# Kernel optimization log

Hardware: AMD Instinct MI355X
Metric: run time of the kernel (lower is better)

## Reference

```python
import jax, jax.numpy as jnp
import numpy as np
import math

VOCAB = 32000
D_MODEL = 1024
N_HEADS = 16
D_FF = 4096
N_LAYERS = 4
MAX_LEN = 2048
BATCH = 2
SEQ = 1024


def _sinusoidal_pe(max_len, d_model):
    pos = np.arange(max_len, dtype=np.float32)[:, None]
    div = np.exp(np.arange(0, d_model, 2, dtype=np.float32) * (-math.log(10000.0) / d_model))
    pe = np.zeros((max_len, d_model), dtype=np.float32)
    pe[:, 0::2] = np.sin(pos * div)
    pe[:, 1::2] = np.cos(pos * div)
    return jnp.asarray(pe)


def setup_inputs() -> dict:
    key = jax.random.key(0)
    ks = jax.random.split(key, 16)
    std = 0.02
    L, d, ff, V = N_LAYERS, D_MODEL, D_FF, VOCAB
    inp = {
        "input_ids": jax.random.randint(ks[0], (BATCH, SEQ), 0, V, dtype=jnp.int32),
        "tok_emb": jax.random.normal(ks[1], (V, d), jnp.float32) * std,
        "pe": _sinusoidal_pe(MAX_LEN, d),
        "Wq": jax.random.normal(ks[2], (L, d, d), jnp.float32) * std,
        "Wk": jax.random.normal(ks[3], (L, d, d), jnp.float32) * std,
        "Wv": jax.random.normal(ks[4], (L, d, d), jnp.float32) * std,
        "Wo": jax.random.normal(ks[5], (L, d, d), jnp.float32) * std,
        "bo": jnp.zeros((L, d), jnp.float32),
        "W1": jax.random.normal(ks[6], (L, d, ff), jnp.float32) * std,
        "b1": jnp.zeros((L, ff), jnp.float32),
        "W2": jax.random.normal(ks[7], (L, ff, d), jnp.float32) * std,
        "b2": jnp.zeros((L, d), jnp.float32),
        "ln1_g": jnp.ones((L, d), jnp.float32),
        "ln1_b": jnp.zeros((L, d), jnp.float32),
        "ln2_g": jnp.ones((L, d), jnp.float32),
        "ln2_b": jnp.zeros((L, d), jnp.float32),
        "lnf_g": jnp.ones((d,), jnp.float32),
        "lnf_b": jnp.zeros((d,), jnp.float32),
        "Whead": jax.random.normal(ks[8], (V, d), jnp.float32) * std,
    }
    return inp


def _layernorm(x, g, b, eps=1e-5):
    mu = jnp.mean(x, axis=-1, keepdims=True)
    var = jnp.var(x, axis=-1, keepdims=True)
    return (x - mu) * jax.lax.rsqrt(var + eps) * g + b


def reference(input_ids, tok_emb, pe, Wq, Wk, Wv, Wo, bo, W1, b1, W2, b2,
              ln1_g, ln1_b, ln2_g, ln2_b, lnf_g, lnf_b, Whead):
    B, S = input_ids.shape
    d, H = D_MODEL, N_HEADS
    dk = d // H
    scale = math.sqrt(dk)

    x = tok_emb[input_ids] * math.sqrt(d) + pe[:S][None, :, :]  # [B,S,d]
    causal = jnp.tril(jnp.ones((S, S), dtype=bool))  # [S,S]

    for l in range(N_LAYERS):
        # --- attention sub-block (pre-LN) ---
        h = _layernorm(x, ln1_g[l], ln1_b[l])
        q = (h @ Wq[l]).reshape(B, S, H, dk).transpose(0, 2, 1, 3)  # [B,H,S,dk]
        k = (h @ Wk[l]).reshape(B, S, H, dk).transpose(0, 2, 1, 3)
        v = (h @ Wv[l]).reshape(B, S, H, dk).transpose(0, 2, 1, 3)
        scores = jnp.einsum('bhqd,bhkd->bhqk', q, k) / scale  # [B,H,S,S]
        scores = jnp.where(causal[None, None], scores, -1e9)
        attn = jax.nn.softmax(scores, axis=-1)
        ctx = jnp.einsum('bhqk,bhkd->bhqd', attn, v)  # [B,H,S,dk]
        ctx = ctx.transpose(0, 2, 1, 3).reshape(B, S, d)
        x = x + ctx @ Wo[l] + bo[l]
        # --- feed-forward sub-block ---
        h = _layernorm(x, ln2_g[l], ln2_b[l])
        x = x + jax.nn.relu(h @ W1[l] + b1[l]) @ W2[l] + b2[l]

    x = _layernorm(x, lnf_g, lnf_b)
    logits = x @ Whead.T  # [B,S,V]
    return logits
```

## Files before the change

kernel.cpp:

```cpp
#include <hip/hip_runtime.h>
#include <stdint.h>

typedef unsigned short u16;
typedef unsigned int   u32;

#define D_MODEL 1024
#define NHEADS  16
#define DKH     64
#define DFF     4096
#define NLAYERS 4
#define BATCH   2
#define SEQ     1024
#define NTOK    (BATCH*SEQ)
#define NVOCAB  32000
#define QKV_LD  3072

typedef __bf16 bf16x8 __attribute__((ext_vector_type(8)));
typedef float  f32x4  __attribute__((ext_vector_type(4)));
typedef u32    u32x4  __attribute__((ext_vector_type(4)));

static __device__ __forceinline__ u16 f2bf(float f){
    union { float f; u32 u; } v; v.f = f;
    return (u16)((v.u + 0x7fffu + ((v.u >> 16) & 1u)) >> 16);
}
static __device__ __forceinline__ u32 pk2(float lo, float hi){
    return (u32)f2bf(lo) | ((u32)f2bf(hi) << 16);
}
static __device__ __forceinline__ bf16x8 ldb8(const u16* p){
    return *reinterpret_cast<const bf16x8*>(p);
}
static __device__ __forceinline__ f32x4 mfma16(bf16x8 a, bf16x8 b, f32x4 c){
    return __builtin_amdgcn_mfma_f32_16x16x32_bf16(a, b, c, 0, 0, 0);
}
static __device__ __forceinline__ void gld16(const void* g, void* l){
    __builtin_amdgcn_global_load_lds((__attribute__((address_space(1))) u32*)g,
                                     (__attribute__((address_space(3))) u32*)l, 16, 0, 0);
}

__global__ __launch_bounds__(256) void k_embed(const int* __restrict__ ids,
        const float* __restrict__ tok, const float* __restrict__ pe,
        float* __restrict__ x){
    int t = blockIdx.x;
    int c = threadIdx.x * 4;
    int id = ids[t];
    int s = t & (SEQ - 1);
    float4 tv = *(const float4*)(tok + (size_t)id * D_MODEL + c);
    float4 pv = *(const float4*)(pe  + (size_t)s  * D_MODEL + c);
    float4 o;
    o.x = tv.x * 32.0f + pv.x;
    o.y = tv.y * 32.0f + pv.y;
    o.z = tv.z * 32.0f + pv.z;
    o.w = tv.w * 32.0f + pv.w;
    *(float4*)(x + (size_t)t * D_MODEL + c) = o;
}

__global__ __launch_bounds__(256) void k_ln(const float* __restrict__ x,
        const float* __restrict__ g, const float* __restrict__ b,
        u16* __restrict__ out){
    int t = blockIdx.x;
    int tid = threadIdx.x;
    float4 v = *(const float4*)(x + (size_t)t * D_MODEL + tid * 4);
    float s  = v.x + v.y + v.z + v.w;
    float ss = v.x*v.x + v.y*v.y + v.z*v.z + v.w*v.w;
    #pragma unroll
    for (int off = 1; off < 64; off <<= 1){
        s  += __shfl_xor(s, off);
        ss += __shfl_xor(ss, off);
    }
    __shared__ float rs[4], rss[4];
    int w = tid >> 6;
    if ((tid & 63) == 0){ rs[w] = s; rss[w] = ss; }
    __syncthreads();
    s  = rs[0] + rs[1] + rs[2] + rs[3];
    ss = rss[0] + rss[1] + rss[2] + rss[3];
    float mu  = s * (1.0f / D_MODEL);
    float var = ss * (1.0f / D_MODEL) - mu * mu;
    float rstd = rsqrtf(var + 1e-5f);
    float4 gg = *(const float4*)(g + tid * 4);
    float4 bb = *(const float4*)(b + tid * 4);
    uint2 pkv;
    pkv.x = pk2((v.x - mu) * rstd * gg.x + bb.x, (v.y - mu) * rstd * gg.y + bb.y);
    pkv.y = pk2((v.z - mu) * rstd * gg.z + bb.z, (v.w - mu) * rstd * gg.w + bb.w);
    *(uint2*)(out + (size_t)t * D_MODEL + tid * 4) = pkv;
}

__global__ __launch_bounds__(256) void k_ln_acc(float* __restrict__ x,
        const float* __restrict__ p0, const float* __restrict__ p1,
        const float* __restrict__ bias,
        const float* __restrict__ g, const float* __restrict__ b,
        u16* __restrict__ out){
    int t = blockIdx.x;
    int tid = threadIdx.x;
    size_t idx = (size_t)t * D_MODEL + tid * 4;
    float4 v  = *(const float4*)(x + idx);
    float4 a0 = *(const float4*)(p0 + idx);
    float4 a1 = *(const float4*)(p1 + idx);
    float4 bv = *(const float4*)(bias + tid * 4);
    v.x += a0.x + a1.x + bv.x;
    v.y += a0.y + a1.y + bv.y;
    v.z += a0.z + a1.z + bv.z;
    v.w += a0.w + a1.w + bv.w;
    *(float4*)(x + idx) = v;
    float s  = v.x + v.y + v.z + v.w;
    float ss = v.x*v.x + v.y*v.y + v.z*v.z + v.w*v.w;
    #pragma unroll
    for (int off = 1; off < 64; off <<= 1){
        s  += __shfl_xor(s, off);
        ss += __shfl_xor(ss, off);
    }
    __shared__ float rs[4], rss[4];
    int w = tid >> 6;
    if ((tid & 63) == 0){ rs[w] = s; rss[w] = ss; }
    __syncthreads();
    s  = rs[0] + rs[1] + rs[2] + rs[3];
    ss = rss[0] + rss[1] + rss[2] + rss[3];
    float mu  = s * (1.0f / D_MODEL);
    float var = ss * (1.0f / D_MODEL) - mu * mu;
    float rstd = rsqrtf(var + 1e-5f);
    float4 gg = *(const float4*)(g + tid * 4);
    float4 bb = *(const float4*)(b + tid * 4);
    uint2 pkv;
    pkv.x = pk2((v.x - mu) * rstd * gg.x + bb.x, (v.y - mu) * rstd * gg.y + bb.y);
    pkv.y = pk2((v.z - mu) * rstd * gg.z + bb.z, (v.w - mu) * rstd * gg.w + bb.w);
    *(uint2*)(out + idx) = pkv;
}

__global__ __launch_bounds__(256) void k_cast(const float* __restrict__ in,
        u16* __restrict__ out){
    size_t i = ((size_t)blockIdx.x * 256 + threadIdx.x) * 8;
    float4 a = *(const float4*)(in + i);
    float4 b = *(const float4*)(in + i + 4);
    u32x4 o;
    o.x = pk2(a.x, a.y); o.y = pk2(a.z, a.w);
    o.z = pk2(b.x, b.y); o.w = pk2(b.z, b.w);
    *(u32x4*)(out + i) = o;
}

__global__ __launch_bounds__(256) void k_tconv_fused(
        const float* __restrict__ Wq, const float* __restrict__ Wk,
        const float* __restrict__ Wv, const float* __restrict__ Wo,
        const float* __restrict__ W1, const float* __restrict__ W2,
        u16* __restrict__ wqkvT, u16* __restrict__ woT,
        u16* __restrict__ w1T,   u16* __restrict__ w2T){
    __shared__ float tile[32][33];
    const int id = blockIdx.x;
    const float* in; u16* outp; int R, C, bx, by;
    if (id < 4096){
        int wsel = id >> 10, t = id & 1023;
        bx = t & 31; by = t >> 5; R = 1024; C = 1024;
        in   = (wsel == 0) ? Wq : (wsel == 1) ? Wk : (wsel == 2) ? Wv : Wo;
        outp = (wsel < 3) ? wqkvT + wsel * 1024 * 1024 : woT;
    } else if (id < 8192){
        int t = id - 4096; bx = t & 127; by = t >> 7;
        R = 1024; C = 4096; in = W1; outp = w1T;
    } else {
        int t = id - 8192; bx = t & 31; by = t >> 5;
        R = 4096; C = 1024; in = W2; outp = w2T;
    }
    const int tx = threadIdx.x & 31, ty = threadIdx.x >> 5;
    #pragma unroll
    for (int i = 0; i < 4; i++){
        int r = by * 32 + ty + i * 8;
        tile[ty + i * 8][tx] = in[(size_t)r * C + bx * 32 + tx];
    }
    __syncthreads();
    #pragma unroll
    for (int i = 0; i < 4; i++){
        int c = bx * 32 + ty + i * 8;
        outp[(size_t)c * R + by * 32 + tx] = f2bf(tile[tx][ty + i * 8]);
    }
}

__global__ __launch_bounds__(256) void k_vt(const u16* __restrict__ qkv,
        u16* __restrict__ vt){
    __shared__ u16 tile[32][33];
    int sb = blockIdx.x;
    int yz = blockIdx.y;
    int db = yz & 1;
    int bh = yz >> 1;
    int b = bh >> 4, h = bh & 15;
    int tx = threadIdx.x & 31, ty = threadIdx.x >> 5;
    #pragma unroll
    for (int i = 0; i < 4; i++){
        int s = sb * 32 + ty + i * 8;
        tile[ty + i * 8][tx] = qkv[(size_t)(b * SEQ + s) * QKV_LD + 2048 + h * DKH + db * 32 + tx];
    }
    __syncthreads();
    #pragma unroll
    for (int i = 0; i < 4; i++){
        int dh = db * 32 + ty + i * 8;
        vt[(size_t)(bh * DKH + dh) * SEQ + sb * 32 + tx] = tile[tx][ty + i * 8];
    }
}

template<bool BIAS, bool RELU, bool OBF16, bool AXISM>
__global__ __launch_bounds__(256, 2) void k_gemm128p(
    const u16* __restrict__ A, const u16* __restrict__ Bt,
    const float* __restrict__ bias,
    float* __restrict__ outF, u16* __restrict__ outH,
    int N, int Kfull, int NXT, int NMT, int NZ)
{
    __shared__ __align__(16) u16 lds[32768];
    const int bid = blockIdx.x;
    const int xcd = bid & 7;
    const int r   = bid >> 3;
    int m_t, n_t, z;
    if constexpr (AXISM) {
        const int mper = NMT >> 3;
        n_t = r % NXT;
        int r2 = r / NXT;
        z = r2 % NZ;
        m_t = xcd * mper + r2 / NZ;
    } else {
        const int nper = NXT >> 3;
        n_t = xcd * nper + r % nper;
        int r2 = r / nper;
        m_t = r2 % NMT;
        z = r2 / NMT;
    }
    const int m0 = m_t * 128;
    const int n0 = n_t * 128;
    const int Kz = Kfull / NZ;
    const int kbeg = z * Kz;
    const int NT = Kz >> 6;

    const int tid  = threadIdx.x;
    const int w    = tid >> 6;
    const int lane = tid & 63;
    const int wr   = w >> 1, wc = w & 1;
    const int lrow = lane & 15, lkg = lane >> 4;

    const int srow = tid >> 3;
    const int ssw  = ((tid & 7) ^ (srow & 7)) * 8;
    const u16* aSrc0 = A  + (size_t)(m0 +  0 + srow) * Kfull + kbeg + ssw;
    const u16* aSrc1 = A  + (size_t)(m0 + 32 + srow) * Kfull + kbeg + ssw;
    const u16* aSrc2 = A  + (size_t)(m0 + 64 + srow) * Kfull + kbeg + ssw;
    const u16* aSrc3 = A  + (size_t)(m0 + 96 + srow) * Kfull + kbeg + ssw;
    const u16* bSrc0 = Bt + (size_t)(n0 +  0 + srow) * Kfull + kbeg + ssw;
    const u16* bSrc1 = Bt + (size_t)(n0 + 32 + srow) * Kfull + kbeg + ssw;
    const u16* bSrc2 = Bt + (size_t)(n0 + 64 + srow) * Kfull + kbeg + ssw;
    const u16* bSrc3 = Bt + (size_t)(n0 + 96 + srow) * Kfull + kbeg + ssw;

    const int sw0 = ((0 + lkg) ^ (lrow & 7)) * 8;
    const int sw1 = ((4 + lkg) ^ (lrow & 7)) * 8;
    const int aBase = (wr * 64 + lrow) * 64;
    const int bBase = (wc * 64 + lrow) * 64 + 8192;

    f32x4 acc[4][4] = {};

    #define STAGE(s, st) do { \
        u16* ab_ = lds + (s) * 16384 + w * 512; \
        const int ko_ = (st) * 64; \
        gld16(aSrc0 + ko_, ab_);              \
        gld16(aSrc1 + ko_, ab_ + 2048);       \
        gld16(aSrc2 + ko_, ab_ + 4096);       \
        gld16(aSrc3 + ko_, ab_ + 6144);       \
        gld16(bSrc0 + ko_, ab_ + 8192);       \
        gld16(bSrc1 + ko_, ab_ + 10240);      \
        gld16(bSrc2 + ko_, ab_ + 12288);      \
        gld16(bSrc3 + ko_, ab_ + 14336);      \
    } while (0)

    STAGE(0, 0);
    STAGE(1, 1);
    asm volatile("s_waitcnt vmcnt(8)" ::: "memory");
    __builtin_amdgcn_s_barrier();
    __builtin_amdgcn_sched_barrier(0);

    for (int t = 0; t < NT; ++t){
        const int s = t & 1;
        const u16* As = lds + s * 16384;

        bf16x8 af0[4], bf0[4];
        #pragma unroll
        for (int i = 0; i < 4; i++) af0[i] = ldb8(As + aBase + i * 1024 + sw0);
        #pragma unroll
        for (int j = 0; j < 4; j++) bf0[j] = ldb8(As + bBase + j * 1024 + sw0);
        __builtin_amdgcn_s_setprio(1);
        #pragma unroll
        for (int i = 0; i < 4; i++)
            #pragma unroll
            for (int j = 0; j < 4; j++)
                acc[i][j] = mfma16(af0[i], bf0[j], acc[i][j]);
        __builtin_amdgcn_s_setprio(0);

        bf16x8 af1[4], bf1[4];
        #pragma unroll
        for (int i = 0; i < 4; i++) af1[i] = ldb8(As + aBase + i * 1024 + sw1);
        #pragma unroll
        for (int j = 0; j < 4; j++) bf1[j] = ldb8(As + bBase + j * 1024 + sw1);
        asm volatile("s_waitcnt lgkmcnt(0)" ::: "memory");
        __builtin_amdgcn_sched_barrier(0);
        __builtin_amdgcn_s_barrier();
        __builtin_amdgcn_sched_barrier(0);

        STAGE(s, (t + 2 < NT) ? t + 2 : NT - 1);

        __builtin_amdgcn_s_setprio(1);
        #pragma unroll
        for (int i = 0; i < 4; i++)
            #pragma unroll
            for (int j = 0; j < 4; j++)
                acc[i][j] = mfma16(af1[i], bf1[j], acc[i][j]);
        __builtin_amdgcn_s_setprio(0);

        asm volatile("s_waitcnt vmcnt(8)" ::: "memory");
        __builtin_amdgcn_s_barrier();
        __builtin_amdgcn_sched_barrier(0);
    }
    #undef STAGE

    float* outFz = outF;
    if (NZ > 1) outFz += (size_t)z * (NMT * 128) * N;

    #pragma unroll
    for (int i = 0; i < 4; i++){
        #pragma unroll
        for (int j = 0; j < 4; j++){
            const int c = n0 + 64 * wc + 16 * j + lrow;
            float bv = 0.0f;
            if constexpr (BIAS) bv = bias[c];
            #pragma unroll
            for (int e = 0; e < 4; e++){
                const int rr = m0 + 64 * wr + 16 * i + lkg * 4 + e;
                float vv = acc[i][j][e] + bv;
                if constexpr (RELU) vv = fmaxf(vv, 0.0f);
                const size_t idx = (size_t)rr * N + c;
                if constexpr (OBF16) outH[idx] = f2bf(vv);
                else                 outFz[idx] = vv;
            }
        }
    }
}

__global__ __launch_bounds__(512, 2) void k_gemm_head256(
    const u16* __restrict__ A, const u16* __restrict__ Bt,
    float* __restrict__ out)
{
    __shared__ __align__(16) u16 lds[65536];
    const int bid = blockIdx.x;
    const int swz = (bid & 7) * 125 + (bid >> 3);
    const int m0 = (swz >> 3) * 256;
    const int n0 = (swz & 7) * 256;

    const int tid  = threadIdx.x;
    const int w    = tid >> 6;
    const int lane = tid & 63;
    const int wr   = w >> 2, wc = w & 3;
    const int lrow = lane & 15, lkg = lane >> 4;

    const int srow = tid >> 3;
    const int ssw  = ((tid & 7) ^ (srow & 7)) * 8;
    const u16* aSrc0 = A  + (size_t)(m0 +   0 + srow) * D_MODEL + ssw;
    const u16* aSrc1 = A  + (size_t)(m0 +  64 + srow) * D_MODEL + ssw;
    const u16* aSrc2 = A  + (size_t)(m0 + 128 + srow) * D_MODEL + ssw;
    const u16* aSrc3 = A  + (size_t)(m0 + 192 + srow) * D_MODEL + ssw;
    const u16* bSrc0 = Bt + (size_t)(n0 +   0 + srow) * D_MODEL + ssw;
    const u16* bSrc1 = Bt + (size_t)(n0 +  64 + srow) * D_MODEL + ssw;
    const u16* bSrc2 = Bt + (size_t)(n0 + 128 + srow) * D_MODEL + ssw;
    const u16* bSrc3 = Bt + (size_t)(n0 + 192 + srow) * D_MODEL + ssw;

    const int sw0 = ((0 + lkg) ^ (lrow & 7)) * 8;
    const int sw1 = ((4 + lkg) ^ (lrow & 7)) * 8;
    const int aBase = (wr * 128 + lrow) * 64;
    const int bBase = (wc * 64  + lrow) * 64;

    f32x4 acc[8][4] = {};

    #define STAGE(s, st) do { \
        u16* ab_ = lds + (s) * 32768 + w * 512; \
        const int ko_ = (st) * 64; \
        gld16(aSrc0 + ko_, ab_);              \
        gld16(aSrc1 + ko_, ab_ + 4096);       \
        gld16(aSrc2 + ko_, ab_ + 8192);       \
        gld16(aSrc3 + ko_, ab_ + 12288);      \
        gld16(bSrc0 + ko_, ab_ + 16384);      \
        gld16(bSrc1 + ko_, ab_ + 20480);      \
        gld16(bSrc2 + ko_, ab_ + 24576);      \
        gld16(bSrc3 + ko_, ab_ + 28672);      \
    } while (0)

    STAGE(0, 0);
    STAGE(1, 1);
    asm volatile("s_waitcnt vmcnt(8)" ::: "memory");
    __builtin_amdgcn_s_barrier();
    __builtin_amdgcn_sched_barrier(0);

    const int NT = D_MODEL / 64;
    for (int t = 0; t < NT; ++t){
        const int s = t & 1;
        const u16* As = lds + s * 32768;
        const u16* Bs = As + 16384;

        bf16x8 af0[8], bf0[4];
        #pragma unroll
        for (int i = 0; i < 8; i++) af0[i] = ldb8(As + aBase + i * 1024 + sw0);
        #pragma unroll
        for (int j = 0; j < 4; j++) bf0[j] = ldb8(Bs + bBase + j * 1024 + sw0);
        __builtin_amdgcn_s_setprio(1);
        #pragma unroll
        for (int i = 0; i < 8; i++)
            #pragma unroll
            for (int j = 0; j < 4; j++)
                acc[i][j] = mfma16(af0[i], bf0[j], acc[i][j]);
        __builtin_amdgcn_s_setprio(0);

        bf16x8 af1[8], bf1[4];
        #pragma unroll
        for (int i = 0; i < 8; i++) af1[i] = ldb8(As + aBase + i * 1024 + sw1);
        #pragma unroll
        for (int j = 0; j < 4; j++) bf1[j] = ldb8(Bs + bBase + j * 1024 + sw1);
        asm volatile("s_waitcnt lgkmcnt(0)" ::: "memory");
        __builtin_amdgcn_sched_barrier(0);
        __builtin_amdgcn_s_barrier();
        __builtin_amdgcn_sched_barrier(0);

        STAGE(s, (t + 2 < NT) ? t + 2 : NT - 1);

        __builtin_amdgcn_s_setprio(1);
        #pragma unroll
        for (int i = 0; i < 8; i++)
            #pragma unroll
            for (int j = 0; j < 4; j++)
                acc[i][j] = mfma16(af1[i], bf1[j], acc[i][j]);
        __builtin_amdgcn_s_setprio(0);

        asm volatile("s_waitcnt vmcnt(8)" ::: "memory");
        __builtin_amdgcn_s_barrier();
        __builtin_amdgcn_sched_barrier(0);
    }
    #undef STAGE

    #pragma unroll
    for (int i = 0; i < 8; i++){
        const int m = m0 + wr * 128 + i * 16 + lkg * 4;
        #pragma unroll
        for (int j = 0; j < 4; j++){
            const int n = n0 + wc * 64 + j * 16 + lrow;
            float4 st;
            st.x = acc[i][j][0]; st.y = acc[i][j][1];
            st.z = acc[i][j][2]; st.w = acc[i][j][3];
            *(float4*)(out + (size_t)n * NVOCAB + m) = st;
        }
    }
}

__global__ __launch_bounds__(256) void k_attn(const u16* __restrict__ qkv,
        const u16* __restrict__ vt, u16* __restrict__ ctx){
    const int wid  = (blockIdx.x << 2) + (threadIdx.x >> 6);
    const int lane = threadIdx.x & 63;
    const int qt = wid & 63;
    const int h  = (wid >> 6) & 15;
    const int b  = wid >> 10;
    const int q0 = qt * 16;
    const int lrow = lane & 15, lkg = lane >> 4;

    __shared__ __align__(16) u16 plds_all[4][16][72];
    u16 (*plds)[72] = plds_all[threadIdx.x >> 6];

    const u16* qbase = qkv + (size_t)(b * SEQ + q0 + lrow) * QKV_LD + h * DKH + 8 * lkg;
    const bf16x8 qf0 = ldb8(qbase);
    const bf16x8 qf1 = ldb8(qbase + 32);

    float mr[4], lsum[4];
    f32x4 acc[4] = {};
    #pragma unroll
    for (int e = 0; e < 4; e++){ mr[e] = -1e30f; lsum[e] = 0.0f; }

    const int nkb = (q0 >> 6) + 1;
    const u16* kbase  = qkv + (size_t)(b * SEQ) * QKV_LD + 1024 + h * DKH;
    const u16* vtbase = vt + (size_t)((b * NHEADS + h) * DKH) * SEQ;

    for (int kb = 0; kb < nkb; ++kb){
        const int kc = kb * 64;
        f32x4 sg[4] = {};
        const u16* kp = kbase + (size_t)(kc + lrow) * QKV_LD + 8 * lkg;
        bf16x8 ka[4], kbv[4];
        #pragma unroll
        for (int g = 0; g < 4; g++){
            const u16* p = kp + (size_t)(16 * g) * QKV_LD;
            ka[g]  = ldb8(p);
            kbv[g] = ldb8(p + 32);
        }
        __builtin_amdgcn_s_setprio(1);
        #pragma unroll
        for (int g = 0; g < 4; g++){
            sg[g] = mfma16(qf0, ka[g],  sg[g]);
            sg[g] = mfma16(qf1, kbv[g], sg[g]);
        }
        __builtin_amdgcn_s_setprio(0);

        #pragma unroll
        for (int e = 0; e < 4; e++){
            const int row = q0 + lkg * 4 + e;
            float v0 = (kc      + lrow > row) ? -1e30f : sg[0][e] * 0.125f;
            float v1 = (kc + 16 + lrow > row) ? -1e30f : sg[1][e] * 0.125f;
            float v2 = (kc + 32 + lrow > row) ? -1e30f : sg[2][e] * 0.125f;
            float v3 = (kc + 48 + lrow > row) ? -1e30f : sg[3][e] * 0.125f;
            float t = fmaxf(fmaxf(v0, v1), fmaxf(v2, v3));
            t = fmaxf(t, __shfl_xor(t, 1));
            t = fmaxf(t, __shfl_xor(t, 2));
            t = fmaxf(t, __shfl_xor(t, 4));
            t = fmaxf(t, __shfl_xor(t, 8));
            const float mn = fmaxf(mr[e], t);
            const float al = __expf(mr[e] - mn);
            const float p0 = __expf(v0 - mn);
            const float p1 = __expf(v1 - mn);
            const float p2 = __expf(v2 - mn);
            const float p3 = __expf(v3 - mn);
            float rsum = (p0 + p1) + (p2 + p3);
            rsum += __shfl_xor(rsum, 1);
            rsum += __shfl_xor(rsum, 2);
            rsum += __shfl_xor(rsum, 4);
            rsum += __shfl_xor(rsum, 8);
            lsum[e] = lsum[e] * al + rsum;
            mr[e] = mn;
            #pragma unroll
            for (int nt = 0; nt < 4; nt++) acc[nt][e] *= al;
            u16* prow = plds[lkg * 4 + e];
            prow[lrow]      = f2bf(p0);
            prow[16 + lrow] = f2bf(p1);
            prow[32 + lrow] = f2bf(p2);
            prow[48 + lrow] = f2bf(p3);
        }
        asm volatile("" ::: "memory");
        const bf16x8 pf0 = ldb8(&plds[lrow][8 * lkg]);
        const bf16x8 pf1 = ldb8(&plds[lrow][32 + 8 * lkg]);
        __builtin_amdgcn_s_setprio(1);
        #pragma unroll
        for (int nt = 0; nt < 4; nt++){
            const u16* vp = vtbase + (size_t)(16 * nt + lrow) * SEQ + kc + 8 * lkg;
            acc[nt] = mfma16(pf0, ldb8(vp),      acc[nt]);
            acc[nt] = mfma16(pf1, ldb8(vp + 32), acc[nt]);
        }
        __builtin_amdgcn_s_setprio(0);
    }
    #pragma unroll
    for (int nt = 0; nt < 4; nt++){
        #pragma unroll
        for (int e = 0; e < 4; e++){
            const int r = q0 + lkg * 4 + e;
            ctx[(size_t)(b * SEQ + r) * D_MODEL + h * DKH + 16 * nt + lrow] =
                f2bf(acc[nt][e] / lsum[e]);
        }
    }
}

extern "C" void kernel_launch(void* const* d_in, const int* in_sizes, int n_in,
                              void* d_out, int out_size, void* d_ws, size_t ws_size,
                              hipStream_t stream){
    const int*   ids  = (const int*)  d_in[0];
    const float* tok  = (const float*)d_in[1];
    const float* pe   = (const float*)d_in[2];
    const float* Wq   = (const float*)d_in[3];
    const float* Wk   = (const float*)d_in[4];
    const float* Wv   = (const float*)d_in[5];
    const float* Wo   = (const float*)d_in[6];
    const float* bo   = (const float*)d_in[7];
    const float* W1   = (const float*)d_in[8];
    const float* b1   = (const float*)d_in[9];
    const float* W2   = (const float*)d_in[10];
    const float* b2   = (const float*)d_in[11];
    const float* ln1g = (const float*)d_in[12];
    const float* ln1b = (const float*)d_in[13];
    const float* ln2g = (const float*)d_in[14];
    const float* ln2b = (const float*)d_in[15];
    const float* lnfg = (const float*)d_in[16];
    const float* lnfb = (const float*)d_in[17];
    const float* Wh   = (const float*)d_in[18];
    float* out = (float*)d_out;

    char* ws = (char*)d_ws;
    size_t off = 0;
    auto alloc = [&](size_t bytes) -> void* {
        void* p = ws + off;
        off += (bytes + 255) & ~(size_t)255;
        return p;
    };
    float* x     = (float*)alloc((size_t)NTOK * D_MODEL * 4);
    u16*   hbuf  = (u16*)  alloc((size_t)NTOK * D_MODEL * 2);
    u16*   qkv   = (u16*)  alloc((size_t)NTOK * QKV_LD  * 2);
    u16*   vt    = (u16*)  alloc((size_t)NTOK * D_MODEL * 2);
    u16*   ctx   = (u16*)  alloc((size_t)NTOK * D_MODEL * 2);
    u16*   f1    = (u16*)  alloc((size_t)NTOK * DFF     * 2);
    float* pbuf  = (float*)alloc((size_t)2 * NTOK * D_MODEL * 4);
    u16*   wqkvT = (u16*)  alloc((size_t)QKV_LD * D_MODEL * 2);
    u16*   woT   = (u16*)  alloc((size_t)D_MODEL * D_MODEL * 2);
    u16*   w1T   = (u16*)  alloc((size_t)DFF * D_MODEL * 2);
    u16*   w2T   = (u16*)  alloc((size_t)D_MODEL * DFF * 2);
    u16*   whB   = (u16*)  alloc((size_t)NVOCAB * D_MODEL * 2);
    float* p1    = pbuf + (size_t)NTOK * D_MODEL;
    (void)ws_size; (void)in_sizes; (void)n_in; (void)out_size;

    k_embed<<<NTOK, 256, 0, stream>>>(ids, tok, pe, x);
    k_cast<<<(NVOCAB * D_MODEL) / (256 * 8), 256, 0, stream>>>(Wh, whB);

    for (int l = 0; l < NLAYERS; l++){
        const size_t wdd = (size_t)l * D_MODEL * D_MODEL;
        const size_t wdf = (size_t)l * D_MODEL * DFF;
        k_tconv_fused<<<12288, 256, 0, stream>>>(
            Wq + wdd, Wk + wdd, Wv + wdd, Wo + wdd, W1 + wdf, W2 + wdf,
            wqkvT, woT, w1T, w2T);

        if (l == 0)
            k_ln<<<NTOK, 256, 0, stream>>>(x, ln1g, ln1b, hbuf);
        else
            k_ln_acc<<<NTOK, 256, 0, stream>>>(x, pbuf, p1, b2 + (l - 1) * D_MODEL,
                ln1g + l * D_MODEL, ln1b + l * D_MODEL, hbuf);

        k_gemm128p<false, false, true, false><<<384, 256, 0, stream>>>(
            hbuf, wqkvT, nullptr, nullptr, qkv, QKV_LD, D_MODEL, 24, 16, 1);
        k_vt<<<dim3(32, 64), 256, 0, stream>>>(qkv, vt);
        k_attn<<<512, 256, 0, stream>>>(qkv, vt, ctx);

        k_gemm128p<false, false, false, true><<<256, 256, 0, stream>>>(
            ctx, woT, nullptr, pbuf, nullptr, D_MODEL, D_MODEL, 8, 16, 2);
        k_ln_acc<<<NTOK, 256, 0, stream>>>(x, pbuf, p1, bo + l * D_MODEL,
            ln2g + l * D_MODEL, ln2b + l * D_MODEL, hbuf);

        k_gemm128p<true, true, true, false><<<512, 256, 0, stream>>>(
            hbuf, w1T, b1 + l * DFF, nullptr, f1, DFF, D_MODEL, 32, 16, 1);
        k_gemm128p<false, false, false, true><<<256, 256, 0, stream>>>(
            f1, w2T, nullptr, pbuf, nullptr, D_MODEL, DFF, 8, 16, 2);
    }

    k_ln_acc<<<NTOK, 256, 0, stream>>>(x, pbuf, p1, b2 + 3 * D_MODEL,
        lnfg, lnfb, hbuf);
    k_gemm_head256<<<1000, 512, 0, stream>>>(whB, hbuf, out);
}
```

Before: 917.2 us.

## Fuse V transpose into QKV GEMM epilogue and split W2 GEMM four ways

The QKV GEMM epilogue now writes the V columns straight into the transposed vt layout as packed bf16 pairs, so the separate k_vt transpose kernel is gone. The W2 GEMM split-K goes from 2 to 4 partitions, launching 512 blocks instead of 256, and the partial-sum buffer grows to match. k_ln_acc is templated on the number of partials it reduces. This removes one kernel launch plus one read and write of V per layer, and gives the K=4096 GEMM more parallelism, at the cost of reading and writing more fp32 partial sums.

```diff
diff --git a/kernel.cpp b/kernel.cpp
--- a/kernel.cpp
+++ b/kernel.cpp
@@ -84,8 +84,9 @@
     *(uint2*)(out + (size_t)t * D_MODEL + tid * 4) = pkv;
 }
 
+template<int NP>
 __global__ __launch_bounds__(256) void k_ln_acc(float* __restrict__ x,
-        const float* __restrict__ p0, const float* __restrict__ p1,
+        const float* __restrict__ pb,
         const float* __restrict__ bias,
         const float* __restrict__ g, const float* __restrict__ b,
         u16* __restrict__ out){
@@ -93,13 +94,13 @@
     int tid = threadIdx.x;
     size_t idx = (size_t)t * D_MODEL + tid * 4;
     float4 v  = *(const float4*)(x + idx);
-    float4 a0 = *(const float4*)(p0 + idx);
-    float4 a1 = *(const float4*)(p1 + idx);
     float4 bv = *(const float4*)(bias + tid * 4);
-    v.x += a0.x + a1.x + bv.x;
-    v.y += a0.y + a1.y + bv.y;
-    v.z += a0.z + a1.z + bv.z;
-    v.w += a0.w + a1.w + bv.w;
+    v.x += bv.x; v.y += bv.y; v.z += bv.z; v.w += bv.w;
+    #pragma unroll
+    for (int p = 0; p < NP; p++){
+        float4 a = *(const float4*)(pb + (size_t)p * NTOK * D_MODEL + idx);
+        v.x += a.x; v.y += a.y; v.z += a.z; v.w += a.w;
+    }
     *(float4*)(x + idx) = v;
     float s  = v.x + v.y + v.z + v.w;
     float ss = v.x*v.x + v.y*v.y + v.z*v.z + v.w*v.w;
@@ -171,33 +172,11 @@
     }
 }
 
-__global__ __launch_bounds__(256) void k_vt(const u16* __restrict__ qkv,
-        u16* __restrict__ vt){
-    __shared__ u16 tile[32][33];
-    int sb = blockIdx.x;
-    int yz = blockIdx.y;
-    int db = yz & 1;
-    int bh = yz >> 1;
-    int b = bh >> 4, h = bh & 15;
-    int tx = threadIdx.x & 31, ty = threadIdx.x >> 5;
-    #pragma unroll
-    for (int i = 0; i < 4; i++){
-        int s = sb * 32 + ty + i * 8;
-        tile[ty + i * 8][tx] = qkv[(size_t)(b * SEQ + s) * QKV_LD + 2048 + h * DKH + db * 32 + tx];
-    }
-    __syncthreads();
-    #pragma unroll
-    for (int i = 0; i < 4; i++){
-        int dh = db * 32 + ty + i * 8;
-        vt[(size_t)(bh * DKH + dh) * SEQ + sb * 32 + tx] = tile[tx][ty + i * 8];
-    }
-}
-
-template<bool BIAS, bool RELU, bool OBF16, bool AXISM>
+template<bool BIAS, bool RELU, bool OBF16, bool AXISM, bool VFUSE>
 __global__ __launch_bounds__(256, 2) void k_gemm128p(
     const u16* __restrict__ A, const u16* __restrict__ Bt,
     const float* __restrict__ bias,
-    float* __restrict__ outF, u16* __restrict__ outH,
+    float* __restrict__ outF, u16* __restrict__ outH, u16* __restrict__ vtOut,
     int N, int Kfull, int NXT, int NMT, int NZ)
 {
     __shared__ __align__(16) u16 lds[32768];
@@ -318,16 +297,26 @@
         #pragma unroll
         for (int j = 0; j < 4; j++){
             const int c = n0 + 64 * wc + 16 * j + lrow;
-            float bv = 0.0f;
-            if constexpr (BIAS) bv = bias[c];
-            #pragma unroll
-            for (int e = 0; e < 4; e++){
-                const int rr = m0 + 64 * wr + 16 * i + lkg * 4 + e;
-                float vv = acc[i][j][e] + bv;
-                if constexpr (RELU) vv = fmaxf(vv, 0.0f);
-                const size_t idx = (size_t)rr * N + c;
-                if constexpr (OBF16) outH[idx] = f2bf(vv);
-                else                 outFz[idx] = vv;
+            if (VFUSE && n0 >= 2048) {
+                const int hv = (c - 2048) >> 6, dh = (c - 2048) & 63;
+                const int r0 = m0 + 64 * wr + 16 * i + lkg * 4;
+                const int bb = r0 >> 10, ss = r0 & 1023;
+                uint2 pv;
+                pv.x = pk2(acc[i][j][0], acc[i][j][1]);
+                pv.y = pk2(acc[i][j][2], acc[i][j][3]);
+                *(uint2*)(vtOut + (((size_t)((bb * 16 + hv) * 64 + dh)) << 10) + ss) = pv;
+            } else {
+                float bv = 0.0f;
+                if constexpr (BIAS) bv = bias[c];
+                #pragma unroll
+                for (int e = 0; e < 4; e++){
+                    const int rr = m0 + 64 * wr + 16 * i + lkg * 4 + e;
+                    float vv = acc[i][j][e] + bv;
+                    if constexpr (RELU) vv = fmaxf(vv, 0.0f);
+                    const size_t idx = (size_t)rr * N + c;
+                    if constexpr (OBF16) outH[idx] = f2bf(vv);
+                    else                 outFz[idx] = vv;
+                }
             }
         }
     }
@@ -583,13 +572,12 @@
     u16*   vt    = (u16*)  alloc((size_t)NTOK * D_MODEL * 2);
     u16*   ctx   = (u16*)  alloc((size_t)NTOK * D_MODEL * 2);
     u16*   f1    = (u16*)  alloc((size_t)NTOK * DFF     * 2);
-    float* pbuf  = (float*)alloc((size_t)2 * NTOK * D_MODEL * 4);
+    float* pbuf  = (float*)alloc((size_t)4 * NTOK * D_MODEL * 4);
     u16*   wqkvT = (u16*)  alloc((size_t)QKV_LD * D_MODEL * 2);
     u16*   woT   = (u16*)  alloc((size_t)D_MODEL * D_MODEL * 2);
     u16*   w1T   = (u16*)  alloc((size_t)DFF * D_MODEL * 2);
     u16*   w2T   = (u16*)  alloc((size_t)D_MODEL * DFF * 2);
     u16*   whB   = (u16*)  alloc((size_t)NVOCAB * D_MODEL * 2);
-    float* p1    = pbuf + (size_t)NTOK * D_MODEL;
     (void)ws_size; (void)in_sizes; (void)n_in; (void)out_size;
 
     k_embed<<<NTOK, 256, 0, stream>>>(ids, tok, pe, x);
@@ -605,26 +593,25 @@
         if (l == 0)
             k_ln<<<NTOK, 256, 0, stream>>>(x, ln1g, ln1b, hbuf);
         else
-            k_ln_acc<<<NTOK, 256, 0, stream>>>(x, pbuf, p1, b2 + (l - 1) * D_MODEL,
+            k_ln_acc<4><<<NTOK, 256, 0, stream>>>(x, pbuf, b2 + (l - 1) * D_MODEL,
                 ln1g + l * D_MODEL, ln1b + l * D_MODEL, hbuf);
 
-        k_gemm128p<false, false, true, false><<<384, 256, 0, stream>>>(
-            hbuf, wqkvT, nullptr, nullptr, qkv, QKV_LD, D_MODEL, 24, 16, 1);
-        k_vt<<<dim3(32, 64), 256, 0, stream>>>(qkv, vt);
+        k_gemm128p<false, false, true, false, true><<<384, 256, 0, stream>>>(
+            hbuf, wqkvT, nullptr, nullptr, qkv, vt, QKV_LD, D_MODEL, 24, 16, 1);
         k_attn<<<512, 256, 0, stream>>>(qkv, vt, ctx);
 
-        k_gemm128p<false, false, false, true><<<256, 256, 0, stream>>>(
-            ctx, woT, nullptr, pbuf, nullptr, D_MODEL, D_MODEL, 8, 16, 2);
-        k_ln_acc<<<NTOK, 256, 0, stream>>>(x, pbuf, p1, bo + l * D_MODEL,
+        k_gemm128p<false, false, false, true, false><<<256, 256, 0, stream>>>(
+            ctx, woT, nullptr, pbuf, nullptr, nullptr, D_MODEL, D_MODEL, 8, 16, 2);
+        k_ln_acc<2><<<NTOK, 256, 0, stream>>>(x, pbuf, bo + l * D_MODEL,
             ln2g + l * D_MODEL, ln2b + l * D_MODEL, hbuf);
 
-        k_gemm128p<true, true, true, false><<<512, 256, 0, stream>>>(
-            hbuf, w1T, b1 + l * DFF, nullptr, f1, DFF, D_MODEL, 32, 16, 1);
-        k_gemm128p<false, false, false, true><<<256, 256, 0, stream>>>(
-            f1, w2T, nullptr, pbuf, nullptr, D_MODEL, DFF, 8, 16, 2);
-    }
-
-    k_ln_acc<<<NTOK, 256, 0, stream>>>(x, pbuf, p1, b2 + 3 * D_MODEL,
+        k_gemm128p<true, true, true, false, false><<<512, 256, 0, stream>>>(
+            hbuf, w1T, b1 + l * DFF, nullptr, f1, nullptr, DFF, D_MODEL, 32, 16, 1);
+        k_gemm128p<false, false, false, true, false><<<512, 256, 0, stream>>>(
+            f1, w2T, nullptr, pbuf, nullptr, nullptr, D_MODEL, DFF, 8, 16, 4);
+    }
+
+    k_ln_acc<4><<<NTOK, 256, 0, stream>>>(x, pbuf, b2 + 3 * D_MODEL,
         lnfg, lnfb, hbuf);
     k_gemm_head256<<<1000, 512, 0, stream>>>(whB, hbuf, out);
 }
```

After: 922.6 us. Within noise of the previous version (+0.6%).
